# Optimization experiments

Measured on AMD Instinct MI355X. Metric: run time of the kernel, lower is better.

Reference implementation:

```python
import jax, jax.numpy as jnp
import numpy as np

# Architecture constants (match init_kwargs)
B = 64          # batch
INPUT = 128     # input_size
SS = 9          # simple_size (V1 kernel)
DIMS = INPUT - SS + 1            # 120, V1 output grid
SN = 8          # simple_number (orientations)
PS = 4          # phis_sfs (phases)
C = SN * PS     # 32 V1 channels
V4K = 8         # v4_size
V4S = 4         # v4_stride
V4D = (DIMS - V4K) // V4S + 1    # 29
ORI = 16        # v4_orientation_number


def _patches(x, k, s):
    """x: [N, H, W] -> [N, oh, ow, k*k]; kernel dim is row-major (kh, kw),
    matching torch .unfold(2,k,s).unfold(3,k,s).view(..., k*k)."""
    p = jax.lax.conv_general_dilated_patches(x[:, None], (k, k), (s, s), 'VALID')
    return jnp.moveaxis(p, 1, -1)  # [N, oh, ow, k*k]


def setup_inputs() -> dict:
    key = jax.random.key(0)
    k0, k1, k2, k3 = jax.random.split(key, 4)
    x = jax.random.normal(k0, (B, 1, INPUT, INPUT), jnp.float32)
    # Unshared (per-location) V1 weights: [C, dims, dims, ss^2]
    simple_weight = jax.random.normal(k1, (C, DIMS, DIMS, SS * SS), jnp.float32) * 0.05
    # Unshared V4 pooling weights: [ORI, SN, v4d, v4d, v4k^2]
    v4_weight = jax.random.normal(k2, (ORI, SN, V4D, V4D, V4K * V4K), jnp.float32) * 0.05
    dec_w = jax.random.normal(k3, (2, ORI * V4D * V4D), jnp.float32) * 0.01
    dec_b = jnp.zeros((2,), jnp.float32)
    return {"x": x, "simple_weight": simple_weight, "v4_weight": v4_weight,
            "dec_w": dec_w, "dec_b": dec_b}


def reference(x, simple_weight, v4_weight, dec_w, dec_b):
    b = x.shape[0]
    # --- V1 locally-connected layer (unfold + per-location weighted sum) ---
    p1 = _patches(x[:, 0], SS, 1)                         # [B, 120, 120, 81]
    v1 = jnp.einsum('bijk,cijk->bcij', p1, simple_weight)  # [B, 32, 120, 120]
    # --- complex-cell pooling over phases (relu then combine phis_sfs) ---
    cplx = jax.nn.relu(v1).reshape(b, SN, PS, DIMS, DIMS).mean(2)  # [B, 8, 120, 120]
    # --- V4 locally-connected pooling per orientation channel ---
    p2 = _patches(cplx.reshape(b * SN, DIMS, DIMS), V4K, V4S)
    p2 = p2.reshape(b, SN, V4D, V4D, V4K * V4K)            # [B, 8, 29, 29, 64]
    v4 = jnp.einsum('bsijk,osijk->boij', p2, v4_weight)    # [B, 16, 29, 29]
    # --- decision readout ---
    flat = v4.reshape(b, -1)                               # [B, 13456]
    return flat @ dec_w.T + dec_b                          # [B, 2]
```

## Files before the change

kernel.cpp:

```cpp
#include <hip/hip_runtime.h>
#include <hip/hip_bf16.h>
#include <stdint.h>

#define B64   64
#define DIMS  120
#define NLOC  (DIMS*DIMS)
#define V4D   29
#define NLOC4 (V4D*V4D)

typedef __attribute__((ext_vector_type(8))) short bf16x8;
typedef __attribute__((ext_vector_type(4))) float f32x4;

__device__ __forceinline__ unsigned short f2bf(float f) {
    unsigned u = __float_as_uint(f);
    u += 0x7fffu + ((u >> 16) & 1u);
    return (unsigned short)(u >> 16);
}

__global__ __launch_bounds__(256) void k0_pack(const float* __restrict__ x,
                                               unsigned short* __restrict__ xrep,
                                               unsigned short* __restrict__ xrepT) {
    __shared__ unsigned short tile[16 * 16 * 64];
    int blk = blockIdx.x;
    int isT = (blk >= 128) ? 1 : 0;
    int b2 = blk - 128 * isT;
    int g = b2 >> 3;
    int fb = (b2 & 7) << 4;
    int tid = threadIdx.x;
    int bb = tid >> 2, c4 = (tid & 3) << 2;
#pragma unroll 4
    for (int rr = 0; rr < 16; ++rr) {
        int row, col;
        if (!isT) { row = 8 * g + rr; col = fb + c4; }
        else      { row = fb + rr;    col = 8 * g + c4; }
        f32x4 v;
        if (row < 128 && col < 128)
            v = *(const f32x4*)(x + ((size_t)bb * 128 + row) * 128 + col);
        else
            v = (f32x4){0.f, 0.f, 0.f, 0.f};
#pragma unroll
        for (int cc = 0; cc < 4; ++cc) {
            int d1 = isT ? rr : (c4 + cc);
            int d2 = isT ? (c4 + cc) : rr;
            tile[(d1 * 16 + d2) * 64 + bb] = f2bf(v[cc]);
        }
    }
    __syncthreads();
    unsigned short* outp = isT ? xrepT : xrep;
    int b = tid & 63;
#pragma unroll
    for (int it = 0; it < 32; ++it) {
        int u = (it * 256 + tid) >> 6;
        int d1 = u & 15, rq = u >> 4;
        bf16x8 pk;
#pragma unroll
        for (int q = 0; q < 8; ++q)
            pk[q] = (short)tile[(d1 * 16 + rq + q) * 64 + b];
        size_t off = ((((size_t)rq * 128 + (fb + d1)) * 16 + g) * 64 + b) * 8;
        *(bf16x8*)(outp + off) = pk;
    }
}

__global__ __launch_bounds__(256) void k1_v1(const unsigned short* __restrict__ xrep,
                                             const unsigned short* __restrict__ xrepT,
                                             const float* __restrict__ sw,
                                             unsigned short* __restrict__ cplx) {
    __shared__ __align__(16) char smraw[4 * 32 * 104 * 2];
    unsigned short* stage = (unsigned short*)smraw;
    float* pool2 = (float*)smraw;

    int tid = threadIdx.x;
    int blk = blockIdx.x;
    int blk2 = (blk & 7) * 450 + (blk >> 3);
    int loc0 = blk2 * 4;

    if (tid < 128) {
        unsigned short* rowp = stage + tid * 104;
#pragma unroll
        for (int z = 81; z < 96; ++z) rowp[z] = 0;
    }
#pragma unroll
    for (int it = 0; it < 11; ++it) {
        int idx = it * 256 + tid;
        if (idx < 2592) {
            int c = idx / 81, r4 = idx - c * 81;
            f32x4 v = *(const f32x4*)(sw + ((size_t)c * NLOC + loc0) * 81 + r4 * 4);
            int posf = r4 * 4;
#pragma unroll
            for (int qq = 0; qq < 4; ++qq) {
                int pp = posf + qq;
                int w2 = 0, e = pp;
                if (e >= 162) { w2 = 2; e -= 162; }
                if (e >= 81)  { w2 += 1; e -= 81; }
                int slot;
                if (e < 72) { int jj = e / 9; slot = (e - 9 * jj) * 8 + jj; }
                else        { slot = e; }
                stage[(w2 * 32 + c) * 104 + slot] = f2bf(v[qq]);
            }
        }
    }
    __syncthreads();

    int w = tid >> 6, l = tid & 63;
    int loc = loc0 + w;
    int i = loc / DIMS, j = loc - i * DIMS;
    int ln = l & 15, t = l >> 4;
    int r = i & 7, g = i >> 3, rc = j & 7, gc = j >> 3;
    const unsigned short* stw = stage + w * 32 * 104;

    f32x4 acc[4][2];
#pragma unroll
    for (int mt = 0; mt < 4; ++mt)
#pragma unroll
        for (int nt = 0; nt < 2; ++nt)
            acc[mt][nt] = (f32x4){0.f, 0.f, 0.f, 0.f};

#pragma unroll
    for (int ks = 0; ks < 3; ++ks) {
        int ch = ks * 4 + t;
        const unsigned short* abase;
        if (ks < 2) {
            int col = j + ch;
            abase = xrep + (((size_t)r * 128 + col) * 16 + g) * 512;
        } else {
            const unsigned short* a0 = xrep + (((size_t)r * 128 + (j + 8)) * 16 + g) * 512;
            int gc2 = gc + ((t >= 2) ? 1 : 0);
            const unsigned short* a1 = xrepT + (((size_t)rc * 128 + (i + 8)) * 16 + gc2) * 512;
            abase = (t == 0) ? a0 : a1;
        }
        bf16x8 a[4];
#pragma unroll
        for (int mt = 0; mt < 4; ++mt)
            a[mt] = *(const bf16x8*)(abase + (size_t)(ln + 16 * mt) * 8);
        bf16x8 bfr[2];
#pragma unroll
        for (int nt = 0; nt < 2; ++nt)
            bfr[nt] = *(const bf16x8*)(stw + (ln + 16 * nt) * 104 + ch * 8);
#pragma unroll
        for (int mt = 0; mt < 4; ++mt)
#pragma unroll
            for (int nt = 0; nt < 2; ++nt)
                acc[mt][nt] = __builtin_amdgcn_mfma_f32_16x16x32_bf16(
                    a[mt], bfr[nt], acc[mt][nt], 0, 0, 0);
    }

    __syncthreads();
    float* pl = pool2 + w * 64 * 9;
#pragma unroll
    for (int mt = 0; mt < 4; ++mt)
#pragma unroll
        for (int nt = 0; nt < 2; ++nt)
#pragma unroll
            for (int reg = 0; reg < 4; ++reg) {
                float v = fmaxf(acc[mt][nt][reg], 0.0f);
                v += __shfl_xor(v, 1, 64);
                v += __shfl_xor(v, 2, 64);
                if ((ln & 3) == 0) {
                    int b = 16 * mt + 4 * t + reg;
                    int s = 4 * nt + (ln >> 2);
                    pl[b * 9 + s] = v * 0.25f;
                }
            }
    __syncthreads();
    bf16x8 po;
#pragma unroll
    for (int s = 0; s < 8; ++s)
        po[s] = (short)f2bf(pl[l * 9 + s]);
    *(bf16x8*)(cplx + (size_t)loc * 512 + l * 8) = po;
}

__global__ __launch_bounds__(256) void k2_v4(const unsigned short* __restrict__ cplx,
                                             const float* __restrict__ vw,
                                             float* __restrict__ v4s) {
    __shared__ __align__(16) char smraw[16384];
    unsigned short* stg2 = (unsigned short*)smraw;
    float* pool = (float*)smraw;

    int tid = threadIdx.x;
    int blk = blockIdx.x;
    int loc = (blk < 840) ? ((blk & 7) * 105 + (blk >> 3)) : 840;
    int oi = loc / V4D, oj = loc - oi * V4D;

#pragma unroll
    for (int it = 0; it < 8; ++it) {
        int idx = it * 256 + tid;
        int row = idx >> 4, p4 = (idx & 15) * 4;
        f32x4 v = *(const f32x4*)(vw + ((size_t)row * NLOC4 + loc) * 64 + p4);
        int o = row >> 3, s = row & 7;
#pragma unroll
        for (int qq = 0; qq < 4; ++qq)
            stg2[((p4 + qq) * 16 + o) * 8 + s] = f2bf(v[qq]);
    }
    __syncthreads();

    int w = tid >> 6, l = tid & 63;
    int ln = l & 15, t = l >> 4;
    f32x4 acc[4];
#pragma unroll
    for (int mt = 0; mt < 4; ++mt) acc[mt] = (f32x4){0.f, 0.f, 0.f, 0.f};

#pragma unroll
    for (int kk = 0; kk < 4; ++kk) {
        int pos = 4 * (w * 4 + kk) + t;
        int kh = pos >> 3, kw = pos & 7;
        int iloc = (oi * 4 + kh) * DIMS + oj * 4 + kw;
        const unsigned short* ab = cplx + (size_t)iloc * 512 + ln * 8;
        bf16x8 a[4];
#pragma unroll
        for (int mt = 0; mt < 4; ++mt)
            a[mt] = *(const bf16x8*)(ab + mt * 128);
        bf16x8 bb = *(const bf16x8*)(stg2 + (pos * 16 + ln) * 8);
#pragma unroll
        for (int mt = 0; mt < 4; ++mt)
            acc[mt] = __builtin_amdgcn_mfma_f32_16x16x32_bf16(a[mt], bb, acc[mt], 0, 0, 0);
    }
    __syncthreads();
#pragma unroll
    for (int mt = 0; mt < 4; ++mt)
#pragma unroll
        for (int reg = 0; reg < 4; ++reg)
            pool[((w * 64) + 16 * mt + 4 * t + reg) * 16 + ln] = acc[mt][reg];
    __syncthreads();
    int o = tid & 15, brow = tid >> 4;
#pragma unroll
    for (int itb = 0; itb < 4; ++itb) {
        int b = brow + 16 * itb;
        float s = pool[(0 * 64 + b) * 16 + o] + pool[(1 * 64 + b) * 16 + o] +
                  pool[(2 * 64 + b) * 16 + o] + pool[(3 * 64 + b) * 16 + o];
        v4s[(size_t)loc * 1024 + b * 16 + o] = s;
    }
}

__global__ __launch_bounds__(256) void k3_dec(const float* __restrict__ v4s,
                                              const float* __restrict__ dw,
                                              const float* __restrict__ db,
                                              float* __restrict__ out) {
    int b = blockIdx.x, tid = threadIdx.x;
    float a0 = 0.f, a1 = 0.f;
    for (int loc = tid; loc < NLOC4; loc += 256) {
        const float* vp = v4s + (size_t)loc * 1024 + b * 16;
#pragma unroll
        for (int o4 = 0; o4 < 4; ++o4) {
            f32x4 v = *(const f32x4*)(vp + o4 * 4);
#pragma unroll
            for (int q = 0; q < 4; ++q) {
                int o = o4 * 4 + q;
                a0 += v[q] * dw[o * NLOC4 + loc];
                a1 += v[q] * dw[16 * NLOC4 + o * NLOC4 + loc];
            }
        }
    }
    __shared__ float r0[256], r1[256];
    r0[tid] = a0; r1[tid] = a1;
    __syncthreads();
    for (int s = 128; s > 0; s >>= 1) {
        if (tid < s) { r0[tid] += r0[tid + s]; r1[tid] += r1[tid + s]; }
        __syncthreads();
    }
    if (tid == 0) {
        out[2 * b + 0] = r0[0] + db[0];
        out[2 * b + 1] = r1[0] + db[1];
    }
}

extern "C" void kernel_launch(void* const* d_in, const int* in_sizes, int n_in,
                              void* d_out, int out_size, void* d_ws, size_t ws_size,
                              hipStream_t stream) {
    const float* x  = (const float*)d_in[0];
    const float* sw = (const float*)d_in[1];
    const float* vw = (const float*)d_in[2];
    const float* dw = (const float*)d_in[3];
    const float* db = (const float*)d_in[4];
    float* out = (float*)d_out;

    char* ws = (char*)d_ws;
    unsigned short* xrep  = (unsigned short*)ws;
    unsigned short* xrepT = (unsigned short*)(ws + 16777216);
    unsigned short* cplx  = (unsigned short*)(ws + 33554432);
    float*          v4s   = (float*)(ws + 48300032);

    k0_pack<<<256, 256, 0, stream>>>(x, xrep, xrepT);
    k1_v1<<<NLOC / 4, 256, 0, stream>>>(xrep, xrepT, sw, cplx);
    k2_v4<<<NLOC4, 256, 0, stream>>>(cplx, vw, v4s);
    k3_dec<<<B64, 256, 0, stream>>>(v4s, dw, db, out);
}
```

Before: 290.4 us.

## Pre-pack V1 weights into an MFMA-ready bf16 layout in a separate kernel

Adds a kernel, launched with one block per location, that converts the fp32 unshared V1 weights to bf16. It writes them to a workspace buffer in the fragment order the MFMA loop reads. The V1 kernel then loads its B fragments straight from that buffer instead of staging and transposing weights through shared memory, which also removes a barrier. The cost is an extra launch and a full bf16 write plus re-read of the weight tensor on every call, on top of the original fp32 read.

```diff
diff --git a/kernel.cpp b/kernel.cpp
--- a/kernel.cpp
+++ b/kernel.cpp
@@ -61,52 +61,61 @@
     }
 }
 
+__global__ __launch_bounds__(256) void k0b_swp(const float* __restrict__ sw,
+                                               unsigned short* __restrict__ swp) {
+    __shared__ __align__(16) unsigned short stg[32 * 104];
+    int tid = threadIdx.x;
+    int loc = blockIdx.x;
+    if (tid < 32) {
+        unsigned short* rp = stg + tid * 104;
+#pragma unroll
+        for (int z = 81; z < 96; ++z) rp[z] = 0;
+    }
+#pragma unroll
+    for (int it = 0; it < 3; ++it) {
+        int idx = it * 256 + tid;
+        if (idx < 640) {
+            int c = idx / 20, r4 = idx - c * 20;
+            f32x4 v = *(const f32x4*)(sw + ((size_t)c * NLOC + loc) * 81 + r4 * 4);
+#pragma unroll
+            for (int qq = 0; qq < 4; ++qq) {
+                int e = r4 * 4 + qq;
+                int kh = e / 9, kw = e - 9 * kh;
+                int slot = (e < 72) ? (kw * 8 + kh) : e;
+                stg[c * 104 + slot] = f2bf(v[qq]);
+            }
+        }
+    }
+    if (tid < 32)
+        stg[tid * 104 + 80] = f2bf(sw[((size_t)tid * NLOC + loc) * 81 + 80]);
+    __syncthreads();
+#pragma unroll
+    for (int it = 0; it < 2; ++it) {
+        int idx = it * 256 + tid;
+        if (idx < 384) {
+            int ch = idx >> 5, c = idx & 31;
+            bf16x8 pk = *(const bf16x8*)(stg + c * 104 + ch * 8);
+            *(bf16x8*)(swp + (((size_t)loc * 12 + ch) * 32 + c) * 8) = pk;
+        }
+    }
+}
+
 __global__ __launch_bounds__(256) void k1_v1(const unsigned short* __restrict__ xrep,
                                              const unsigned short* __restrict__ xrepT,
-                                             const float* __restrict__ sw,
+                                             const unsigned short* __restrict__ swp,
                                              unsigned short* __restrict__ cplx) {
-    __shared__ __align__(16) char smraw[4 * 32 * 104 * 2];
-    unsigned short* stage = (unsigned short*)smraw;
-    float* pool2 = (float*)smraw;
-
+    __shared__ float pool2[4 * 64 * 9];
     int tid = threadIdx.x;
     int blk = blockIdx.x;
     int blk2 = (blk & 7) * 450 + (blk >> 3);
     int loc0 = blk2 * 4;
-
-    if (tid < 128) {
-        unsigned short* rowp = stage + tid * 104;
-#pragma unroll
-        for (int z = 81; z < 96; ++z) rowp[z] = 0;
-    }
-#pragma unroll
-    for (int it = 0; it < 11; ++it) {
-        int idx = it * 256 + tid;
-        if (idx < 2592) {
-            int c = idx / 81, r4 = idx - c * 81;
-            f32x4 v = *(const f32x4*)(sw + ((size_t)c * NLOC + loc0) * 81 + r4 * 4);
-            int posf = r4 * 4;
-#pragma unroll
-            for (int qq = 0; qq < 4; ++qq) {
-                int pp = posf + qq;
-                int w2 = 0, e = pp;
-                if (e >= 162) { w2 = 2; e -= 162; }
-                if (e >= 81)  { w2 += 1; e -= 81; }
-                int slot;
-                if (e < 72) { int jj = e / 9; slot = (e - 9 * jj) * 8 + jj; }
-                else        { slot = e; }
-                stage[(w2 * 32 + c) * 104 + slot] = f2bf(v[qq]);
-            }
-        }
-    }
-    __syncthreads();
 
     int w = tid >> 6, l = tid & 63;
     int loc = loc0 + w;
     int i = loc / DIMS, j = loc - i * DIMS;
     int ln = l & 15, t = l >> 4;
     int r = i & 7, g = i >> 3, rc = j & 7, gc = j >> 3;
-    const unsigned short* stw = stage + w * 32 * 104;
+    const unsigned short* swl = swp + (size_t)loc * 12 * 32 * 8;
 
     f32x4 acc[4][2];
 #pragma unroll
@@ -135,7 +144,7 @@
         bf16x8 bfr[2];
 #pragma unroll
         for (int nt = 0; nt < 2; ++nt)
-            bfr[nt] = *(const bf16x8*)(stw + (ln + 16 * nt) * 104 + ch * 8);
+            bfr[nt] = *(const bf16x8*)(swl + ((size_t)ch * 32 + ln + 16 * nt) * 8);
 #pragma unroll
         for (int mt = 0; mt < 4; ++mt)
 #pragma unroll
@@ -144,7 +153,6 @@
                     a[mt], bfr[nt], acc[mt][nt], 0, 0, 0);
     }
 
-    __syncthreads();
     float* pl = pool2 + w * 64 * 9;
 #pragma unroll
     for (int mt = 0; mt < 4; ++mt)
@@ -278,9 +286,11 @@
     unsigned short* xrepT = (unsigned short*)(ws + 16777216);
     unsigned short* cplx  = (unsigned short*)(ws + 33554432);
     float*          v4s   = (float*)(ws + 48300032);
+    unsigned short* swp   = (unsigned short*)(ws + 51744768);
 
     k0_pack<<<256, 256, 0, stream>>>(x, xrep, xrepT);
-    k1_v1<<<NLOC / 4, 256, 0, stream>>>(xrep, xrepT, sw, cplx);
+    k0b_swp<<<NLOC, 256, 0, stream>>>(sw, swp);
+    k1_v1<<<NLOC / 4, 256, 0, stream>>>(xrep, xrepT, swp, cplx);
     k2_v4<<<NLOC4, 256, 0, stream>>>(cplx, vw, v4s);
     k3_dec<<<B64, 256, 0, stream>>>(v4s, dw, db, out);
 }
```

New measurement: 317.0 us. 1.09x slower.
